# Optimization experiments

Hardware: AMD Instinct MI355X
Metric: run time of the kernel (lower is better)

## Reference

```python
import jax, jax.numpy as jnp
import numpy as np

B, N, D, E, HEADS = 2, 256, 768, 8192, 8
HD = D // HEADS
EPS = 1e-5


def _lin(x, w, b):
    return x @ w.T + b


def setup_inputs() -> dict:
    key = jax.random.key(0)
    ks = iter(jax.random.split(key, 64))

    def W(*s):
        return jax.random.normal(next(ks), s, jnp.float32) * 0.02

    inp = {
        "node_embeddings": jax.random.normal(next(ks), (B, N, D), jnp.float32),
        "edge_weights": jax.random.uniform(next(ks), (E,), jnp.float32),
        "edge_indices": jax.random.randint(next(ks), (E, 2), 0, N, jnp.int32),
        # object classifier: D->D->D//2->8
        "oc_w1": W(D, D), "oc_b1": jnp.zeros((D,), jnp.float32),
        "oc_w2": W(D // 2, D), "oc_b2": jnp.zeros((D // 2,), jnp.float32),
        "oc_w3": W(8, D // 2), "oc_b3": jnp.zeros((8,), jnp.float32),
        # importance predictor: D->D//2->D//4->1
        "ip_w1": W(D // 2, D), "ip_b1": jnp.zeros((D // 2,), jnp.float32),
        "ip_w2": W(D // 4, D // 2), "ip_b2": jnp.zeros((D // 4,), jnp.float32),
        "ip_w3": W(1, D // 4), "ip_b3": jnp.zeros((1,), jnp.float32),
        # relation classifier: 2D->D->D//2->8
        "rc_w1": W(D, 2 * D), "rc_b1": jnp.zeros((D,), jnp.float32),
        "rc_w2": W(D // 2, D), "rc_b2": jnp.zeros((D // 2,), jnp.float32),
        "rc_w3": W(8, D // 2), "rc_b3": jnp.zeros((8,), jnp.float32),
        # attention in/out projections
        "attn_in_w": W(3 * D, D), "attn_in_b": jnp.zeros((3 * D,), jnp.float32),
        "attn_out_w": W(D, D), "attn_out_b": jnp.zeros((D,), jnp.float32),
    }
    for l in range(3):
        inp[f"gnn{l}_ws"] = W(D, D)
        inp[f"gnn{l}_bs"] = jnp.zeros((D,), jnp.float32)
        inp[f"gnn{l}_wn"] = W(D, D)
        inp[f"gnn{l}_bn"] = jnp.zeros((D,), jnp.float32)
        inp[f"gnn{l}_g"] = jnp.ones((D,), jnp.float32)
        inp[f"gnn{l}_beta"] = jnp.zeros((D,), jnp.float32)
    return inp


def reference(node_embeddings, edge_weights, edge_indices,
              oc_w1, oc_b1, oc_w2, oc_b2, oc_w3, oc_b3,
              ip_w1, ip_b1, ip_w2, ip_b2, ip_w3, ip_b3,
              rc_w1, rc_b1, rc_w2, rc_b2, rc_w3, rc_b3,
              attn_in_w, attn_in_b, attn_out_w, attn_out_b,
              gnn0_ws, gnn0_bs, gnn0_wn, gnn0_bn, gnn0_g, gnn0_beta,
              gnn1_ws, gnn1_bs, gnn1_wn, gnn1_bn, gnn1_g, gnn1_beta,
              gnn2_ws, gnn2_bs, gnn2_wn, gnn2_bn, gnn2_g, gnn2_beta):
    x = node_embeddings  # [B,N,D]
    src, tgt = edge_indices[:, 0], edge_indices[:, 1]

    # object classifier (dropout is identity in eval)
    h = jax.nn.relu(_lin(x, oc_w1, oc_b1))
    h = jax.nn.relu(_lin(h, oc_w2, oc_b2))
    object_cls = jax.nn.softmax(_lin(h, oc_w3, oc_b3), axis=-1)

    # importance predictor
    h = jax.nn.relu(_lin(x, ip_w1, ip_b1))
    h = jax.nn.relu(_lin(h, ip_w2, ip_b2))
    importance = jax.nn.sigmoid(_lin(h, ip_w3, ip_b3))

    # 3 GNN layers: self-linear + weighted scatter-add neighbor aggregation
    g = x
    layers = [(gnn0_ws, gnn0_bs, gnn0_wn, gnn0_bn, gnn0_g, gnn0_beta),
              (gnn1_ws, gnn1_bs, gnn1_wn, gnn1_bn, gnn1_g, gnn1_beta),
              (gnn2_ws, gnn2_bs, gnn2_wn, gnn2_bn, gnn2_g, gnn2_beta)]
    for ws, bs, wn, bn, gm, bt in layers:
        self_f = _lin(g, ws, bs)
        # vectorized scatter-add: agg[b,tgt] += w_e * g[b,src]
        agg = jnp.zeros_like(g).at[:, tgt, :].add(edge_weights[None, :, None] * g[:, src, :])
        neigh_f = _lin(agg, wn, bn)
        o = jax.nn.relu(self_f + neigh_f)
        mu = o.mean(axis=-1, keepdims=True)
        var = o.var(axis=-1, keepdims=True)  # biased, as torch LayerNorm
        g = gm * (o - mu) / jnp.sqrt(var + EPS) + bt

    # multi-head self-attention (torch MultiheadAttention, batch_first)
    qkv = _lin(g, attn_in_w, attn_in_b)  # [B,N,3D]
    q, k, v = jnp.split(qkv, 3, axis=-1)

    def heads(t):
        return t.reshape(B, N, HEADS, HD).transpose(0, 2, 1, 3)  # [B,H,N,hd]

    q, k, v = heads(q), heads(k), heads(v)
    scores = jnp.einsum('bhqd,bhkd->bhqk', q, k) / jnp.sqrt(jnp.float32(HD))
    attn = jax.nn.softmax(scores, axis=-1)
    ctx = jnp.einsum('bhqk,bhkd->bhqd', attn, v).transpose(0, 2, 1, 3).reshape(B, N, D)
    attended = _lin(ctx, attn_out_w, attn_out_b)  # [B,N,D]
    attn_weights = attn.mean(axis=1)  # torch averages heads -> [B,N,N]

    # all O(N^2) upper-triangular pairs, same (i<j) row-major order as the loop
    ii, jj = np.triu_indices(N, k=1)
    pair = jnp.concatenate([attended[:, ii, :], attended[:, jj, :]], axis=-1)  # [B,P,2D]
    h = jax.nn.relu(_lin(pair, rc_w1, rc_b1))
    h = jax.nn.relu(_lin(h, rc_w2, rc_b2))
    relation = jax.nn.softmax(_lin(h, rc_w3, rc_b3), axis=-1)  # [B,P,8]

    return (object_cls, relation, importance, attended, attn_weights)
```

## Files before the change

kernel.cpp:

```cpp
#include <hip/hip_runtime.h>
#include <hip/hip_bf16.h>

typedef __bf16 bf16;
typedef __bf16 bf16x4 __attribute__((ext_vector_type(4)));
typedef __bf16 bf16x8 __attribute__((ext_vector_type(8)));
typedef float  f32x4  __attribute__((ext_vector_type(4)));

#define NB 2
#define NN 256
#define DD 768
#define EE 8192
#define NPAIR 32640

__device__ inline float wred_sum(float v) {
#pragma unroll
  for (int o = 32; o > 0; o >>= 1) v += __shfl_down(v, o, 64);
  return v;
}
__device__ inline float wred_max(float v) {
#pragma unroll
  for (int o = 32; o > 0; o >>= 1) v = fmaxf(v, __shfl_down(v, o, 64));
  return v;
}

typedef const __attribute__((address_space(1))) void GASV;
typedef __attribute__((address_space(3))) void LASV;
__device__ __forceinline__ void async_cp16(const void* g, void* l) {
  __builtin_amdgcn_global_load_lds((GASV*)g, (LASV*)l, 16, 0, 0);
}

struct CJob { const float* s; bf16* d; int n; };
struct CJobs { CJob j[15]; };
__global__ __launch_bounds__(256) void preamble(
    CJobs jobs, const int* __restrict__ eidx, int* __restrict__ estart,
    int* __restrict__ bucket, int2* __restrict__ pairs)
{
  int by = blockIdx.y, t = threadIdx.x;
  if (by < 15) {
    const CJob jb = jobs.j[by];
    int nv = jb.n >> 2;
    for (int i = blockIdx.x * 256 + t; i < nv; i += gridDim.x * 256) {
      float4 v = ((const float4*)jb.s)[i];
      bf16x4 pk = { (bf16)v.x, (bf16)v.y, (bf16)v.z, (bf16)v.w };
      *(bf16x4*)(jb.d + 4 * i) = pk;
    }
  } else if (by == 15) {
    if (blockIdx.x != 0) return;
    __shared__ int tg[EE];
    __shared__ int cnt[256];
    __shared__ int sst[257];
    cnt[t] = 0;
    for (int e = t; e < EE; e += 256) tg[e] = eidx[2 * e + 1];
    __syncthreads();
    for (int e = t; e < EE; e += 256) atomicAdd(&cnt[tg[e]], 1);
    __syncthreads();
    if (t == 0) { int s = 0; for (int i = 0; i < 256; ++i) { sst[i] = s; s += cnt[i]; } sst[256] = s; }
    __syncthreads();
    estart[t] = sst[t];
    if (t == 0) estart[256] = sst[256];
    cnt[t] = sst[t];
    __syncthreads();
    for (int e = t; e < EE; e += 256) {
      int p = atomicAdd(&cnt[tg[e]], 1);
      bucket[p] = e;
    }
  } else {
#pragma unroll
    for (int u = 0; u < 2; ++u) {
      int i = blockIdx.x + u * 128;
      if (i < 255) {
        int off = i * 255 - (i * (i - 1)) / 2;
        for (int j = i + 1 + t; j < NN; j += 256)
          pairs[off + (j - i - 1)] = make_int2(i, j);
      }
    }
  }
}

__device__ __forceinline__ void lin_core(
    int m0, int n0, const bf16* __restrict__ X, const bf16* __restrict__ W,
    int ldw, int wofs, const float* __restrict__ bias, const float* __restrict__ addF,
    bf16* __restrict__ outB, float* __restrict__ outF, int N, int K, int act)
{
  int lane = threadIdx.x & 63, lr = lane & 15, lq = lane >> 4;
  const bf16* xrow = X + (size_t)(m0 + lr) * K;
  const bf16* wbase = W + (size_t)wofs;
  f32x4 acc[2] = {};
  for (int k = 0; k < K; k += 32) {
    bf16x8 a = *(const bf16x8*)(xrow + k + lq * 8);
    bf16x8 b0 = *(const bf16x8*)(wbase + (size_t)(n0 + lr) * ldw + k + lq * 8);
    bf16x8 b1 = *(const bf16x8*)(wbase + (size_t)(n0 + 16 + lr) * ldw + k + lq * 8);
    acc[0] = __builtin_amdgcn_mfma_f32_16x16x32_bf16(a, b0, acc[0], 0, 0, 0);
    acc[1] = __builtin_amdgcn_mfma_f32_16x16x32_bf16(a, b1, acc[1], 0, 0, 0);
  }
#pragma unroll
  for (int t = 0; t < 2; ++t) {
    int col = n0 + t * 16 + lr;
    float bv = bias ? bias[col] : 0.0f;
#pragma unroll
    for (int r = 0; r < 4; ++r) {
      int row = m0 + lq * 4 + r;
      size_t o = (size_t)row * N + col;
      float v = acc[t][r] + bv;
      if (addF) v += addF[o];
      if (act) v = fmaxf(v, 0.0f);
      if (outB) outB[o] = (bf16)v;
      if (outF) outF[o] = v;
    }
  }
}

__global__ __launch_bounds__(128) void linear_mfma(
    const bf16* __restrict__ X, const bf16* __restrict__ W, int ldw, int wofs,
    const float* __restrict__ bias, const float* __restrict__ addF,
    bf16* __restrict__ outB, float* __restrict__ outF,
    int N, int K, int act)
{
  int wave = threadIdx.x >> 6;
  lin_core((blockIdx.x * 2 + wave) * 16, blockIdx.y * 32,
           X, W, ldw, wofs, bias, addF, outB, outF, N, K, act);
}

struct LinJob {
  const bf16* X; const bf16* W; int ldw; int wofs;
  const float* bias; const float* addF; bf16* outB; float* outF;
  int N, K, act, gy;
};
__global__ __launch_bounds__(128) void linear_mfma2(LinJob j0, LinJob j1)
{
  LinJob j = blockIdx.z ? j1 : j0;
  if ((int)blockIdx.y >= j.gy) return;
  int wave = threadIdx.x >> 6;
  lin_core((blockIdx.x * 2 + wave) * 16, blockIdx.y * 32,
           j.X, j.W, j.ldw, j.wofs, j.bias, j.addF, j.outB, j.outF, j.N, j.K, j.act);
}

__global__ __launch_bounds__(256) void gnn_stage1(
    const bf16* __restrict__ g, const bf16* __restrict__ ws, const float* __restrict__ bs,
    float* __restrict__ selfF,
    const float* __restrict__ ew, const int* __restrict__ eidx,
    const int* __restrict__ estart, const int* __restrict__ bucket, bf16* __restrict__ agg)
{
  int bid = blockIdx.x, t = threadIdx.x;
  if (bid < 192) {
    int wave = t >> 6;
    lin_core(((bid & 7) * 4 + wave) * 16, (bid >> 3) * 32,
             g, ws, 768, 0, bs, nullptr, nullptr, selfF, 768, 768, 0);
    return;
  }
  __shared__ int   ssrc[256];
  __shared__ float sw[256];
  int e0 = bid - 192;
  int tgt = e0 & 255, b = e0 >> 8;
  int s = estart[tgt], e = estart[tgt + 1];
  s = max(0, min(s, EE));
  e = max(s, min(e, EE));
  const bf16* gb = g + (size_t)b * NN * DD;
  float a0 = 0, a1 = 0, a2 = 0, a3 = 0;
  for (int base = s; base < e; base += 256) {
    int nchunk = min(256, e - base);
    if (t < nchunk) {
      int eid = bucket[base + t];
      eid = max(0, min(eid, EE - 1));
      ssrc[t] = eidx[2 * eid] & (NN - 1);
      sw[t] = ew[eid];
    }
    __syncthreads();
    if (t < 192) {
      for (int q = 0; q < nchunk; ++q) {
        float w = sw[q];
        bf16x4 v = *(const bf16x4*)(gb + (size_t)ssrc[q] * DD + 4 * t);
        a0 += w * (float)v[0]; a1 += w * (float)v[1];
        a2 += w * (float)v[2]; a3 += w * (float)v[3];
      }
    }
    __syncthreads();
  }
  if (t < 192) {
    bf16x4 o = { (bf16)a0, (bf16)a1, (bf16)a2, (bf16)a3 };
    *(bf16x4*)(agg + ((size_t)b * NN + tgt) * DD + 4 * t) = o;
  }
}

__global__ __launch_bounds__(256) void layer_norm(
    const float* __restrict__ o, const float* __restrict__ gm,
    const float* __restrict__ bt, bf16* __restrict__ gout)
{
  __shared__ float red[8];
  int row = blockIdx.x, t = threadIdx.x;
  const float* orow = o + (size_t)row * DD;
  float v0 = orow[t], v1 = orow[t + 256], v2 = orow[t + 512];
  float s = v0 + v1 + v2;
  float q = v0 * v0 + v1 * v1 + v2 * v2;
  float ws_ = wred_sum(s), wq = wred_sum(q);
  if ((t & 63) == 0) { red[t >> 6] = ws_; red[4 + (t >> 6)] = wq; }
  __syncthreads();
  float S = red[0] + red[1] + red[2] + red[3];
  float Q = red[4] + red[5] + red[6] + red[7];
  float mu = S * (1.0f / 768.0f);
  float var = Q * (1.0f / 768.0f) - mu * mu;
  float rstd = rsqrtf(var + 1e-5f);
  bf16* gr = gout + (size_t)row * DD;
  gr[t]       = (bf16)(gm[t]       * (v0 - mu) * rstd + bt[t]);
  gr[t + 256] = (bf16)(gm[t + 256] * (v1 - mu) * rstd + bt[t + 256]);
  gr[t + 512] = (bf16)(gm[t + 512] * (v2 - mu) * rstd + bt[t + 512]);
}

__global__ __launch_bounds__(256) void attn_kernel(
    const bf16* __restrict__ qkv, float* __restrict__ aw, bf16* __restrict__ ctx)
{
  __shared__ float qs[96];
  __shared__ float ps[256];
  __shared__ float part[192];
  __shared__ float red[8];
  int qi = blockIdx.x, h = blockIdx.y, b = blockIdx.z, t = threadIdx.x;
  const bf16* qrow = qkv + ((size_t)(b * NN + qi)) * 2304 + h * 96;
  if (t < 96) qs[t] = (float)qrow[t];
  __syncthreads();
  const bf16* krow = qkv + ((size_t)(b * NN + t)) * 2304 + 768 + h * 96;
  float s = 0;
#pragma unroll
  for (int i = 0; i < 12; ++i) {
    bf16x8 kv = *(const bf16x8*)(krow + 8 * i);
#pragma unroll
    for (int j = 0; j < 8; ++j) s += qs[8 * i + j] * (float)kv[j];
  }
  s *= 0.10206207261596577f;
  float wm = wred_max(s);
  if ((t & 63) == 0) red[t >> 6] = wm;
  __syncthreads();
  float MX = fmaxf(fmaxf(red[0], red[1]), fmaxf(red[2], red[3]));
  float e = expf(s - MX);
  float wsum = wred_sum(e);
  if ((t & 63) == 0) red[4 + (t >> 6)] = wsum;
  __syncthreads();
  float SUM = red[4] + red[5] + red[6] + red[7];
  float p = e / SUM;
  ps[t] = p;
  atomicAdd(&aw[((size_t)(b * NN + qi)) * NN + t], p * 0.125f);
  __syncthreads();
  if (t < 192) {
    int d = t % 96, half = t / 96;
    const bf16* vbase = qkv + (size_t)b * NN * 2304 + 1536 + h * 96 + d;
    float a0 = 0, a1 = 0, a2 = 0, a3 = 0;
    int k0 = half * 128;
    for (int k = k0; k < k0 + 128; k += 4) {
      a0 += ps[k]     * (float)vbase[(size_t)k * 2304];
      a1 += ps[k + 1] * (float)vbase[(size_t)(k + 1) * 2304];
      a2 += ps[k + 2] * (float)vbase[(size_t)(k + 2) * 2304];
      a3 += ps[k + 3] * (float)vbase[(size_t)(k + 3) * 2304];
    }
    part[t] = (a0 + a1) + (a2 + a3);
  }
  __syncthreads();
  if (t < 96)
    ctx[((size_t)(b * NN + qi)) * DD + h * 96 + t] = (bf16)(part[t] + part[t + 96]);
}

__global__ __launch_bounds__(256) void fc8_softmax(
    const bf16* __restrict__ h, const float* __restrict__ w,
    const float* __restrict__ bias, float* __restrict__ out)
{
  __shared__ float sw3[8 * 384];
  int t = threadIdx.x;
  for (int i = t; i < 8 * 384; i += 256) sw3[i] = w[i];
  __syncthreads();
  int wave = t >> 6, lane = t & 63;
  int k0 = lane * 6;
#pragma unroll
  for (int i = 0; i < 4; ++i) {
    int r = blockIdx.x * 16 + wave * 4 + i;
    const bf16* hr = h + (size_t)r * 384;
    float hv[6];
#pragma unroll
    for (int j = 0; j < 6; ++j) hv[j] = (float)hr[k0 + j];
    float lg[8];
#pragma unroll
    for (int c = 0; c < 8; ++c) {
      float p = 0;
#pragma unroll
      for (int j = 0; j < 6; ++j) p += hv[j] * sw3[c * 384 + k0 + j];
      lg[c] = wred_sum(p);
    }
    if (lane == 0) {
      float mx = lg[0] + bias[0];
#pragma unroll
      for (int c = 0; c < 8; ++c) { lg[c] += bias[c]; mx = fmaxf(mx, lg[c]); }
      float ex[8], sum = 0;
#pragma unroll
      for (int c = 0; c < 8; ++c) { ex[c] = expf(lg[c] - mx); sum += ex[c]; }
      float inv = 1.0f / sum;
#pragma unroll
      for (int c = 0; c < 8; ++c) out[(size_t)r * 8 + c] = ex[c] * inv;
    }
  }
}

__global__ __launch_bounds__(256) void small_heads(
    const bf16* __restrict__ hOC, const float* __restrict__ w3, const float* __restrict__ b3,
    float* __restrict__ outOC,
    const bf16* __restrict__ hIP, const float* __restrict__ w1, const float* __restrict__ b1,
    float* __restrict__ outIP)
{
  int t = threadIdx.x;
  int wave = t >> 6, lane = t & 63;
  if (blockIdx.x < 32) {
    __shared__ float sw3[8 * 384];
    for (int i = t; i < 8 * 384; i += 256) sw3[i] = w3[i];
    __syncthreads();
    int k0 = lane * 6;
#pragma unroll
    for (int i = 0; i < 4; ++i) {
      int r = blockIdx.x * 16 + wave * 4 + i;
      const bf16* hr = hOC + (size_t)r * 384;
      float hv[6];
#pragma unroll
      for (int j = 0; j < 6; ++j) hv[j] = (float)hr[k0 + j];
      float lg[8];
#pragma unroll
      for (int c = 0; c < 8; ++c) {
        float p = 0;
#pragma unroll
        for (int j = 0; j < 6; ++j) p += hv[j] * sw3[c * 384 + k0 + j];
        lg[c] = wred_sum(p);
      }
      if (lane == 0) {
        float mx = lg[0] + b3[0];
#pragma unroll
        for (int c = 0; c < 8; ++c) { lg[c] += b3[c]; mx = fmaxf(mx, lg[c]); }
        float ex[8], sum = 0;
#pragma unroll
        for (int c = 0; c < 8; ++c) { ex[c] = expf(lg[c] - mx); sum += ex[c]; }
        float inv = 1.0f / sum;
#pragma unroll
        for (int c = 0; c < 8; ++c) outOC[(size_t)r * 8 + c] = ex[c] * inv;
      }
    }
  } else {
    __shared__ float sw1[192];
    if (t < 192) sw1[t] = w1[t];
    __syncthreads();
    int k0 = lane * 3;
#pragma unroll
    for (int i = 0; i < 4; ++i) {
      int r = (blockIdx.x - 32) * 16 + wave * 4 + i;
      const bf16* hr = hIP + (size_t)r * 192;
      float p = (float)hr[k0] * sw1[k0] + (float)hr[k0 + 1] * sw1[k0 + 1]
              + (float)hr[k0 + 2] * sw1[k0 + 2];
      float s = wred_sum(p);
      if (lane == 0) outIP[r] = 1.0f / (1.0f + expf(-(s + b1[0])));
    }
  }
}

__global__ __launch_bounds__(256) void h2_gemm(
    const bf16* __restrict__ Af, const bf16* __restrict__ Bf,
    const bf16* __restrict__ w2, const float* __restrict__ b2,
    const int2* __restrict__ pairs, bf16* __restrict__ h2)
{
  __shared__ bf16x8 sh1[512];
  __shared__ bf16x8 sw2[768];
  __shared__ int rA[128], rB[128];
  int tid = threadIdx.x;
  int r0 = blockIdx.x * 128;
  int bb = (r0 >= NPAIR) ? 1 : 0;
  int n0 = blockIdx.y * 192;
  if (tid < 128) {
    int2 ij = pairs[r0 - bb * NPAIR + tid];
    rA[tid] = (bb * NN + ij.x) * DD;
    rB[tid] = (bb * NN + ij.y) * DD;
  }
  __syncthreads();
  int hrow = tid >> 1, hp = (tid & 1) * 2;
  const bf16* ar = Af + rA[hrow] + hp * 8;
  const bf16* br = Bf + rB[hrow] + hp * 8;
  int hslot = ((hrow >> 4) << 6) + (hp << 4) + (hrow & 15);
  int srow[3], spl[3];
#pragma unroll
  for (int q = 0; q < 3; ++q) {
    int a = q * 256 + tid;
    srow[q] = ((a >> 6) << 4) + (a & 15);
    spl[q] = (a >> 4) & 3;
  }
  int wave = tid >> 6, lane = tid & 63, lr = lane & 15, lq = lane >> 4;
  int wr = wave >> 1, wc = wave & 1;
  f32x4 acc[4][6] = {};
  for (int k0 = 0; k0 < 768; k0 += 32) {
#pragma unroll
    for (int q = 0; q < 3; ++q)
      async_cp16(w2 + (size_t)(n0 + srow[q]) * 768 + k0 + spl[q] * 8,
                 (char*)sw2 + (q * 256 + tid) * 16);
    bf16x8 a0 = *(const bf16x8*)(ar + k0);
    bf16x8 a1 = *(const bf16x8*)(ar + k0 + 8);
    bf16x8 b0 = *(const bf16x8*)(br + k0);
    bf16x8 b1 = *(const bf16x8*)(br + k0 + 8);
    bf16x8 h0, h1v;
#pragma unroll
    for (int j = 0; j < 8; ++j) {
      h0[j]  = (bf16)fmaxf((float)a0[j] + (float)b0[j], 0.f);
      h1v[j] = (bf16)fmaxf((float)a1[j] + (float)b1[j], 0.f);
    }
    sh1[hslot] = h0;
    sh1[hslot + 16] = h1v;
    __syncthreads();
    bf16x8 af[4], bfr[6];
#pragma unroll
    for (int rf = 0; rf < 4; ++rf)
      af[rf] = sh1[(wr * 4 + rf) * 64 + lq * 16 + lr];
#pragma unroll
    for (int cf = 0; cf < 6; ++cf)
      bfr[cf] = sw2[(wc * 6 + cf) * 64 + lq * 16 + lr];
#pragma unroll
    for (int rf = 0; rf < 4; ++rf)
#pragma unroll
      for (int cf = 0; cf < 6; ++cf)
        acc[rf][cf] = __builtin_amdgcn_mfma_f32_16x16x32_bf16(af[rf], bfr[cf], acc[rf][cf], 0, 0, 0);
    __syncthreads();
  }
#pragma unroll
  for (int cf = 0; cf < 6; ++cf) {
    int col = n0 + wc * 96 + cf * 16 + lr;
    float bv2 = b2[col];
#pragma unroll
    for (int rf = 0; rf < 4; ++rf)
#pragma unroll
      for (int r = 0; r < 4; ++r) {
        int prow = r0 + wr * 64 + rf * 16 + lq * 4 + r;
        h2[(size_t)prow * 384 + col] = (bf16)fmaxf(acc[rf][cf][r] + bv2, 0.f);
      }
  }
}

extern "C" void kernel_launch(void* const* d_in, const int* in_sizes, int n_in,
                              void* d_out, int out_size, void* d_ws, size_t ws_size,
                              hipStream_t stream)
{
  (void)in_sizes; (void)n_in; (void)out_size; (void)ws_size;
  const float* x    = (const float*)d_in[0];
  const float* ew   = (const float*)d_in[1];
  const int*   eidx = (const int*)d_in[2];
  const float* oc_w1 = (const float*)d_in[3];  const float* oc_b1 = (const float*)d_in[4];
  const float* oc_w2 = (const float*)d_in[5];  const float* oc_b2 = (const float*)d_in[6];
  const float* oc_w3 = (const float*)d_in[7];  const float* oc_b3 = (const float*)d_in[8];
  const float* ip_w1 = (const float*)d_in[9];  const float* ip_b1 = (const float*)d_in[10];
  const float* ip_w2 = (const float*)d_in[11]; const float* ip_b2 = (const float*)d_in[12];
  const float* ip_w3 = (const float*)d_in[13]; const float* ip_b3 = (const float*)d_in[14];
  const float* rc_w1 = (const float*)d_in[15]; const float* rc_b1 = (const float*)d_in[16];
  const float* rc_w2 = (const float*)d_in[17]; const float* rc_b2 = (const float*)d_in[18];
  const float* rc_w3 = (const float*)d_in[19]; const float* rc_b3 = (const float*)d_in[20];
  const float* at_iw = (const float*)d_in[21]; const float* at_ib = (const float*)d_in[22];
  const float* at_ow = (const float*)d_in[23]; const float* at_ob = (const float*)d_in[24];

  float* out = (float*)d_out;
  float* out_oc  = out;
  float* out_rel = out + 4096;
  float* out_imp = out + 526336;
  float* out_att = out + 526848;
  float* out_aw  = out + 920064;

  char* wp = (char*)d_ws;
  auto alloc = [&](size_t bytes) { char* p = wp; wp += (bytes + 255) & ~(size_t)255; return p; };
  bf16* h2B  = (bf16*)alloc((size_t)(2 * NPAIR) * 384 * 2);
  float* selfF = (float*)alloc((size_t)512 * 768 * 4);
  float* oBuf  = (float*)alloc((size_t)512 * 768 * 4);
  bf16* AfB  = (bf16*)alloc((size_t)512 * 768 * 2);
  bf16* BfB  = (bf16*)alloc((size_t)512 * 768 * 2);
  bf16* xb   = (bf16*)alloc((size_t)512 * 768 * 2);
  bf16* g0   = (bf16*)alloc((size_t)512 * 768 * 2);
  bf16* g1   = (bf16*)alloc((size_t)512 * 768 * 2);
  bf16* hA   = (bf16*)alloc((size_t)512 * 768 * 2);
  bf16* hB   = (bf16*)alloc((size_t)512 * 384 * 2);
  bf16* hI1  = (bf16*)alloc((size_t)512 * 384 * 2);
  bf16* hI2  = (bf16*)alloc((size_t)512 * 192 * 2);
  bf16* aggB = (bf16*)alloc((size_t)512 * 768 * 2);
  bf16* qkv  = (bf16*)alloc((size_t)512 * 2304 * 2);
  bf16* ctx  = (bf16*)alloc((size_t)512 * 768 * 2);
  bf16* attB = (bf16*)alloc((size_t)512 * 768 * 2);
  bf16* w_oc1 = (bf16*)alloc((size_t)768 * 768 * 2);
  bf16* w_oc2 = (bf16*)alloc((size_t)384 * 768 * 2);
  bf16* w_ip1 = (bf16*)alloc((size_t)384 * 768 * 2);
  bf16* w_ip2 = (bf16*)alloc((size_t)192 * 384 * 2);
  bf16* w_rc1 = (bf16*)alloc((size_t)768 * 1536 * 2);
  bf16* w_rc2 = (bf16*)alloc((size_t)384 * 768 * 2);
  bf16* w_aiw = (bf16*)alloc((size_t)2304 * 768 * 2);
  bf16* w_aow = (bf16*)alloc((size_t)768 * 768 * 2);
  bf16* w_gnn[6];
  for (int i = 0; i < 6; ++i) w_gnn[i] = (bf16*)alloc((size_t)768 * 768 * 2);
  int2* pairs = (int2*)alloc((size_t)NPAIR * 8);
  int* estart = (int*)alloc(257 * 4);
  int* bucket = (int*)alloc((size_t)EE * 4);

  dim3 blk(256);
  dim3 blk128(128);

  CJobs cj;
  cj.j[0]  = { x,     xb,    512 * 768 };
  cj.j[1]  = { oc_w1, w_oc1, 768 * 768 };
  cj.j[2]  = { oc_w2, w_oc2, 384 * 768 };
  cj.j[3]  = { ip_w1, w_ip1, 384 * 768 };
  cj.j[4]  = { ip_w2, w_ip2, 192 * 384 };
  cj.j[5]  = { rc_w1, w_rc1, 768 * 1536 };
  cj.j[6]  = { rc_w2, w_rc2, 384 * 768 };
  cj.j[7]  = { at_iw, w_aiw, 2304 * 768 };
  cj.j[8]  = { at_ow, w_aow, 768 * 768 };
  for (int l = 0; l < 3; ++l) {
    cj.j[9 + 2 * l]  = { (const float*)d_in[25 + l * 6 + 0], w_gnn[2 * l],     768 * 768 };
    cj.j[10 + 2 * l] = { (const float*)d_in[25 + l * 6 + 2], w_gnn[2 * l + 1], 768 * 768 };
  }
  hipMemsetAsync(out_aw, 0, (size_t)NB * NN * NN * 4, stream);
  preamble<<<dim3(128, 17), blk, 0, stream>>>(cj, eidx, estart, bucket, pairs);

  {
    LinJob a = { xb, w_oc1, 768, 0, oc_b1, nullptr, hA,  nullptr, 768, 768, 1, 24 };
    LinJob b = { xb, w_ip1, 768, 0, ip_b1, nullptr, hI1, nullptr, 384, 768, 1, 12 };
    linear_mfma2<<<dim3(16, 24, 2), blk128, 0, stream>>>(a, b);
  }
  {
    LinJob a = { hA,  w_oc2, 768, 0, oc_b2, nullptr, hB,  nullptr, 384, 768, 1, 12 };
    LinJob b = { hI1, w_ip2, 384, 0, ip_b2, nullptr, hI2, nullptr, 192, 384, 1, 6 };
    linear_mfma2<<<dim3(16, 12, 2), blk128, 0, stream>>>(a, b);
  }
  small_heads<<<64, blk, 0, stream>>>(hB, oc_w3, oc_b3, out_oc, hI2, ip_w3, ip_b3, out_imp);

  const bf16* gcur = xb;
  bf16* gbufs[2] = { g0, g1 };
  for (int l = 0; l < 3; ++l) {
    const float* bs_ = (const float*)d_in[25 + l * 6 + 1];
    const float* bn_ = (const float*)d_in[25 + l * 6 + 3];
    const float* gm_ = (const float*)d_in[25 + l * 6 + 4];
    const float* bt_ = (const float*)d_in[25 + l * 6 + 5];
    gnn_stage1<<<704, blk, 0, stream>>>(gcur, w_gnn[2 * l], bs_, selfF, ew, eidx, estart, bucket, aggB);
    linear_mfma<<<dim3(16, 24), blk128, 0, stream>>>(aggB, w_gnn[2 * l + 1], 768, 0, bn_, selfF, nullptr, oBuf, 768, 768, 1);
    layer_norm<<<512, blk, 0, stream>>>(oBuf, gm_, bt_, gbufs[l & 1]);
    gcur = gbufs[l & 1];
  }

  linear_mfma<<<dim3(16, 72), blk128, 0, stream>>>(gcur, w_aiw, 768, 0, at_ib, nullptr, qkv, nullptr, 2304, 768, 0);
  attn_kernel<<<dim3(256, 8, 2), blk, 0, stream>>>(qkv, out_aw, ctx);
  linear_mfma<<<dim3(16, 24), blk128, 0, stream>>>(ctx, w_aow, 768, 0, at_ob, nullptr, attB, out_att, 768, 768, 0);

  {
    LinJob a = { attB, w_rc1, 1536, 0,   rc_b1,  nullptr, AfB, nullptr, 768, 768, 0, 24 };
    LinJob b = { attB, w_rc1, 1536, 768, nullptr, nullptr, BfB, nullptr, 768, 768, 0, 24 };
    linear_mfma2<<<dim3(16, 24, 2), blk128, 0, stream>>>(a, b);
  }
  h2_gemm<<<dim3(510, 2), blk, 0, stream>>>(AfB, BfB, w_rc2, rc_b2, pairs, h2B);
  fc8_softmax<<<4080, blk, 0, stream>>>(h2B, rc_w3, rc_b3, out_rel);
}
```

Baseline: 511.0 us.

## Fuse GNN neighbor GEMM with LayerNorm and fold rc_w3 into pair GEMM epilogue

Replaces the per-layer neighbor linear plus separate layer_norm with one gnn_stage2 kernel that does the MFMA GEMM, bias, self-term, ReLU and LayerNorm in registers, using 32 blocks of 16 rows each. The relation head's final 384->8 projection now runs inside h2_gemm's epilogue through a small MFMA over an LDS-staged tile, writing four partial fp32 logit slices. A lightweight relsoftmax kernel sums these and applies the softmax. This removes the large bf16 h2 intermediate (~50MB round trip) and the fp32 oBuf traffic. The cost is a low-parallelism GNN GEMM with only 32 blocks that re-read weights from global memory, plus bf16 rounding of h2 before the last projection.

```diff
diff --git a/kernel.cpp b/kernel.cpp
--- a/kernel.cpp
+++ b/kernel.cpp
@@ -15,11 +15,6 @@
 __device__ inline float wred_sum(float v) {
 #pragma unroll
   for (int o = 32; o > 0; o >>= 1) v += __shfl_down(v, o, 64);
-  return v;
-}
-__device__ inline float wred_max(float v) {
-#pragma unroll
-  for (int o = 32; o > 0; o >>= 1) v = fmaxf(v, __shfl_down(v, o, 64));
   return v;
 }
 
@@ -182,28 +177,66 @@
   }
 }
 
-__global__ __launch_bounds__(256) void layer_norm(
-    const float* __restrict__ o, const float* __restrict__ gm,
+__global__ __launch_bounds__(256) void gnn_stage2(
+    const bf16* __restrict__ agg, const bf16* __restrict__ wn, const float* __restrict__ bn,
+    const float* __restrict__ selfF, const float* __restrict__ gm,
     const float* __restrict__ bt, bf16* __restrict__ gout)
 {
-  __shared__ float red[8];
-  int row = blockIdx.x, t = threadIdx.x;
-  const float* orow = o + (size_t)row * DD;
-  float v0 = orow[t], v1 = orow[t + 256], v2 = orow[t + 512];
-  float s = v0 + v1 + v2;
-  float q = v0 * v0 + v1 * v1 + v2 * v2;
-  float ws_ = wred_sum(s), wq = wred_sum(q);
-  if ((t & 63) == 0) { red[t >> 6] = ws_; red[4 + (t >> 6)] = wq; }
-  __syncthreads();
-  float S = red[0] + red[1] + red[2] + red[3];
-  float Q = red[4] + red[5] + red[6] + red[7];
-  float mu = S * (1.0f / 768.0f);
-  float var = Q * (1.0f / 768.0f) - mu * mu;
-  float rstd = rsqrtf(var + 1e-5f);
-  bf16* gr = gout + (size_t)row * DD;
-  gr[t]       = (bf16)(gm[t]       * (v0 - mu) * rstd + bt[t]);
-  gr[t + 256] = (bf16)(gm[t + 256] * (v1 - mu) * rstd + bt[t + 256]);
-  gr[t + 512] = (bf16)(gm[t + 512] * (v2 - mu) * rstd + bt[t + 512]);
+  __shared__ float red[4][4][4][2];
+  int tid = threadIdx.x;
+  int wave = tid >> 6, lane = tid & 63, lr = lane & 15, lq = lane >> 4;
+  int m0 = blockIdx.x * 16;
+  const bf16* xrow = agg + (size_t)(m0 + lr) * 768;
+  f32x4 acc[12] = {};
+  for (int k = 0; k < 768; k += 32) {
+    bf16x8 a = *(const bf16x8*)(xrow + k + lq * 8);
+#pragma unroll
+    for (int cf = 0; cf < 12; ++cf) {
+      bf16x8 b = *(const bf16x8*)(wn + (size_t)(wave * 192 + cf * 16 + lr) * 768 + k + lq * 8);
+      acc[cf] = __builtin_amdgcn_mfma_f32_16x16x32_bf16(a, b, acc[cf], 0, 0, 0);
+    }
+  }
+  float v[12][4];
+  float s[4] = {0, 0, 0, 0}, q[4] = {0, 0, 0, 0};
+#pragma unroll
+  for (int cf = 0; cf < 12; ++cf) {
+    int col = wave * 192 + cf * 16 + lr;
+    float bv = bn[col];
+#pragma unroll
+    for (int r = 0; r < 4; ++r) {
+      int row = m0 + lq * 4 + r;
+      float x = fmaxf(acc[cf][r] + bv + selfF[(size_t)row * 768 + col], 0.f);
+      v[cf][r] = x;
+      s[r] += x; q[r] += x * x;
+    }
+  }
+#pragma unroll
+  for (int r = 0; r < 4; ++r) {
+#pragma unroll
+    for (int m = 1; m < 16; m <<= 1) {
+      s[r] += __shfl_xor(s[r], m, 64);
+      q[r] += __shfl_xor(q[r], m, 64);
+    }
+  }
+  if (lr == 0) {
+#pragma unroll
+    for (int r = 0; r < 4; ++r) { red[wave][lq][r][0] = s[r]; red[wave][lq][r][1] = q[r]; }
+  }
+  __syncthreads();
+#pragma unroll
+  for (int r = 0; r < 4; ++r) {
+    float S = red[0][lq][r][0] + red[1][lq][r][0] + red[2][lq][r][0] + red[3][lq][r][0];
+    float Q = red[0][lq][r][1] + red[1][lq][r][1] + red[2][lq][r][1] + red[3][lq][r][1];
+    float mu = S * (1.0f / 768.0f);
+    float var = Q * (1.0f / 768.0f) - mu * mu;
+    float rstd = rsqrtf(var + 1e-5f);
+    int row = m0 + lq * 4 + r;
+#pragma unroll
+    for (int cf = 0; cf < 12; ++cf) {
+      int col = wave * 192 + cf * 16 + lr;
+      gout[(size_t)row * 768 + col] = (bf16)(gm[col] * (v[cf][r] - mu) * rstd + bt[col]);
+    }
+  }
 }
 
 __global__ __launch_bounds__(256) void attn_kernel(
@@ -226,7 +259,9 @@
     for (int j = 0; j < 8; ++j) s += qs[8 * i + j] * (float)kv[j];
   }
   s *= 0.10206207261596577f;
-  float wm = wred_max(s);
+  float wm = s;
+#pragma unroll
+  for (int o = 32; o > 0; o >>= 1) wm = fmaxf(wm, __shfl_down(wm, o, 64));
   if ((t & 63) == 0) red[t >> 6] = wm;
   __syncthreads();
   float MX = fmaxf(fmaxf(red[0], red[1]), fmaxf(red[2], red[3]));
@@ -257,45 +292,6 @@
     ctx[((size_t)(b * NN + qi)) * DD + h * 96 + t] = (bf16)(part[t] + part[t + 96]);
 }
 
-__global__ __launch_bounds__(256) void fc8_softmax(
-    const bf16* __restrict__ h, const float* __restrict__ w,
-    const float* __restrict__ bias, float* __restrict__ out)
-{
-  __shared__ float sw3[8 * 384];
-  int t = threadIdx.x;
-  for (int i = t; i < 8 * 384; i += 256) sw3[i] = w[i];
-  __syncthreads();
-  int wave = t >> 6, lane = t & 63;
-  int k0 = lane * 6;
-#pragma unroll
-  for (int i = 0; i < 4; ++i) {
-    int r = blockIdx.x * 16 + wave * 4 + i;
-    const bf16* hr = h + (size_t)r * 384;
-    float hv[6];
-#pragma unroll
-    for (int j = 0; j < 6; ++j) hv[j] = (float)hr[k0 + j];
-    float lg[8];
-#pragma unroll
-    for (int c = 0; c < 8; ++c) {
-      float p = 0;
-#pragma unroll
-      for (int j = 0; j < 6; ++j) p += hv[j] * sw3[c * 384 + k0 + j];
-      lg[c] = wred_sum(p);
-    }
-    if (lane == 0) {
-      float mx = lg[0] + bias[0];
-#pragma unroll
-      for (int c = 0; c < 8; ++c) { lg[c] += bias[c]; mx = fmaxf(mx, lg[c]); }
-      float ex[8], sum = 0;
-#pragma unroll
-      for (int c = 0; c < 8; ++c) { ex[c] = expf(lg[c] - mx); sum += ex[c]; }
-      float inv = 1.0f / sum;
-#pragma unroll
-      for (int c = 0; c < 8; ++c) out[(size_t)r * 8 + c] = ex[c] * inv;
-    }
-  }
-}
-
 __global__ __launch_bounds__(256) void small_heads(
     const bf16* __restrict__ hOC, const float* __restrict__ w3, const float* __restrict__ b3,
     float* __restrict__ outOC,
@@ -356,7 +352,8 @@
 __global__ __launch_bounds__(256) void h2_gemm(
     const bf16* __restrict__ Af, const bf16* __restrict__ Bf,
     const bf16* __restrict__ w2, const float* __restrict__ b2,
-    const int2* __restrict__ pairs, bf16* __restrict__ h2)
+    const float* __restrict__ w3, const int2* __restrict__ pairs,
+    float* __restrict__ logP)
 {
   __shared__ bf16x8 sh1[512];
   __shared__ bf16x8 sw2[768];
@@ -417,18 +414,70 @@
         acc[rf][cf] = __builtin_amdgcn_mfma_f32_16x16x32_bf16(af[rf], bfr[cf], acc[rf][cf], 0, 0, 0);
     __syncthreads();
   }
-#pragma unroll
-  for (int cf = 0; cf < 6; ++cf) {
-    int col = n0 + wc * 96 + cf * 16 + lr;
-    float bv2 = b2[col];
-#pragma unroll
-    for (int rf = 0; rf < 4; ++rf)
+  char* zone = (wave < 2) ? ((char*)sw2 + wave * 3328)
+                          : ((char*)sh1 + (wave - 2) * 3328);
+  bf16x8 w3f[3];
+#pragma unroll
+  for (int ks = 0; ks < 3; ++ks) {
+    bf16x8 f = {};
+    if (lr < 8) {
+      const float* wsrc = w3 + lr * 384 + n0 + wc * 96 + ks * 32 + lq * 8;
+#pragma unroll
+      for (int j = 0; j < 8; ++j) f[j] = (bf16)wsrc[j];
+    }
+    w3f[ks] = f;
+  }
+  float* lp = logP + (size_t)((n0 >= 192 ? 2 : 0) + wc) * 65280 * 8;
+  bf16* zb = (bf16*)zone;
+#pragma unroll
+  for (int rf = 0; rf < 4; ++rf) {
+#pragma unroll
+    for (int cf = 0; cf < 6; ++cf) {
+      int col = n0 + wc * 96 + cf * 16 + lr;
+      float bv2 = b2[col];
+#pragma unroll
+      for (int r = 0; r < 4; ++r)
+        zb[(lq * 4 + r) * 104 + cf * 16 + lr] = (bf16)fmaxf(acc[rf][cf][r] + bv2, 0.f);
+    }
+    f32x4 lacc = {};
+#pragma unroll
+    for (int ks = 0; ks < 3; ++ks) {
+      bf16x8 afr = *(const bf16x8*)(zone + lr * 208 + ks * 64 + lq * 16);
+      lacc = __builtin_amdgcn_mfma_f32_16x16x32_bf16(afr, w3f[ks], lacc, 0, 0, 0);
+    }
+    if (lr < 8) {
 #pragma unroll
       for (int r = 0; r < 4; ++r) {
-        int prow = r0 + wr * 64 + rf * 16 + lq * 4 + r;
-        h2[(size_t)prow * 384 + col] = (bf16)fmaxf(acc[rf][cf][r] + bv2, 0.f);
+        int grow = r0 + wr * 64 + rf * 16 + lq * 4 + r;
+        lp[(size_t)grow * 8 + lr] = lacc[r];
       }
-  }
+    }
+  }
+}
+
+__global__ __launch_bounds__(256) void relsoftmax(
+    const float* __restrict__ logP, const float* __restrict__ b3,
+    float* __restrict__ out)
+{
+  int row = blockIdx.x * 256 + threadIdx.x;
+  float lg[8];
+#pragma unroll
+  for (int c = 0; c < 8; ++c) lg[c] = b3[c];
+#pragma unroll
+  for (int p = 0; p < 4; ++p) {
+    const float* lp = logP + ((size_t)p * 65280 + row) * 8;
+#pragma unroll
+    for (int c = 0; c < 8; ++c) lg[c] += lp[c];
+  }
+  float mx = lg[0];
+#pragma unroll
+  for (int c = 1; c < 8; ++c) mx = fmaxf(mx, lg[c]);
+  float ex[8], sum = 0;
+#pragma unroll
+  for (int c = 0; c < 8; ++c) { ex[c] = expf(lg[c] - mx); sum += ex[c]; }
+  float inv = 1.0f / sum;
+#pragma unroll
+  for (int c = 0; c < 8; ++c) out[(size_t)row * 8 + c] = ex[c] * inv;
 }
 
 extern "C" void kernel_launch(void* const* d_in, const int* in_sizes, int n_in,
@@ -460,9 +509,8 @@
 
   char* wp = (char*)d_ws;
   auto alloc = [&](size_t bytes) { char* p = wp; wp += (bytes + 255) & ~(size_t)255; return p; };
-  bf16* h2B  = (bf16*)alloc((size_t)(2 * NPAIR) * 384 * 2);
+  float* logP  = (float*)alloc((size_t)4 * 65280 * 8 * 4);
   float* selfF = (float*)alloc((size_t)512 * 768 * 4);
-  float* oBuf  = (float*)alloc((size_t)512 * 768 * 4);
   bf16* AfB  = (bf16*)alloc((size_t)512 * 768 * 2);
   bf16* BfB  = (bf16*)alloc((size_t)512 * 768 * 2);
   bf16* xb   = (bf16*)alloc((size_t)512 * 768 * 2);
@@ -530,8 +578,7 @@
     const float* gm_ = (const float*)d_in[25 + l * 6 + 4];
     const float* bt_ = (const float*)d_in[25 + l * 6 + 5];
     gnn_stage1<<<704, blk, 0, stream>>>(gcur, w_gnn[2 * l], bs_, selfF, ew, eidx, estart, bucket, aggB);
-    linear_mfma<<<dim3(16, 24), blk128, 0, stream>>>(aggB, w_gnn[2 * l + 1], 768, 0, bn_, selfF, nullptr, oBuf, 768, 768, 1);
-    layer_norm<<<512, blk, 0, stream>>>(oBuf, gm_, bt_, gbufs[l & 1]);
+    gnn_stage2<<<32, blk, 0, stream>>>(aggB, w_gnn[2 * l + 1], bn_, selfF, gm_, bt_, gbufs[l & 1]);
     gcur = gbufs[l & 1];
   }
 
@@ -544,6 +591,6 @@
     LinJob b = { attB, w_rc1, 1536, 768, nullptr, nullptr, BfB, nullptr, 768, 768, 0, 24 };
     linear_mfma2<<<dim3(16, 24, 2), blk128, 0, stream>>>(a, b);
   }
-  h2_gemm<<<dim3(510, 2), blk, 0, stream>>>(AfB, BfB, w_rc2, rc_b2, pairs, h2B);
-  fc8_softmax<<<4080, blk, 0, stream>>>(h2B, rc_w3, rc_b3, out_rel);
-}
+  h2_gemm<<<dim3(510, 2), blk, 0, stream>>>(AfB, BfB, w_rc2, rc_b2, rc_w3, pairs, logP);
+  relsoftmax<<<255, blk, 0, stream>>>(logP, rc_b3, out_rel);
+}
```

After: 559.2 us. +9.4%, slower.
